# Performance work log

Hardware: AMD Instinct MI355X
Metric: run time of the kernel (lower is better)

## Reference

```python
import jax, jax.numpy as jnp
import numpy as np

H = 3  # heads
NEG_SLOPE = 0.2


def gat_conv(x, edge_index, W, a_src, a_dst, bias):
    # PyG GATConv: add self loops, per-head linear, edge attention, segment softmax over dst.
    N = x.shape[0]
    C = a_src.shape[1]
    loop = jnp.arange(N)
    src = jnp.concatenate([edge_index[0], loop])
    dst = jnp.concatenate([edge_index[1], loop])
    h = (x @ W).reshape(N, H, C)                      # [N,H,C]
    s_src = jnp.sum(h * a_src, axis=-1)               # [N,H]
    s_dst = jnp.sum(h * a_dst, axis=-1)               # [N,H]
    e = jax.nn.leaky_relu(s_src[src] + s_dst[dst], NEG_SLOPE)  # [E,H]
    m = jax.ops.segment_max(e, dst, num_segments=N)   # every node has a self loop -> finite
    e = jnp.exp(e - m[dst])
    denom = jax.ops.segment_sum(e, dst, num_segments=N)
    alpha = e / (denom[dst] + 1e-16)                  # [E,H]
    out = jax.ops.segment_sum(alpha[:, :, None] * h[src], dst, num_segments=N)  # [N,H,C]
    return out.reshape(N, H * C) + bias


def mlp(x, w1, b1, w2, b2):
    return jax.nn.gelu(x @ w1 + b1, approximate=False) @ w2 + b2


def glorot(k, shape):
    fan_in, fan_out = shape[-2], shape[-1]
    lim = np.sqrt(6.0 / (fan_in + fan_out))
    return jax.random.uniform(k, shape, jnp.float32, -lim, lim)


def setup_inputs() -> dict:
    key = jax.random.key(0)
    ks = jax.random.split(key, 24)
    N, E, F, C, HID = 50000, 800000, 256, 64, 128
    inp = {
        "x_st": jax.random.normal(ks[0], (N, F), jnp.float32),
        "edge_index_st": jax.random.randint(ks[1], (2, E), 0, N, jnp.int32),
        "x_sc": jax.random.normal(ks[2], (N, F), jnp.float32),
        "edge_index_sc": jax.random.randint(ks[3], (2, E), 0, N, jnp.int32),
    }
    for i, tag in enumerate(["st", "sc"]):
        o = 4 + i * 10
        inp[f"w_gat_{tag}"] = glorot(ks[o], (F, H * C))
        inp[f"a_src_{tag}"] = glorot(ks[o + 1], (H, C)) * 0.1
        inp[f"a_dst_{tag}"] = glorot(ks[o + 2], (H, C)) * 0.1
        inp[f"b_gat_{tag}"] = jnp.zeros((H * C,), jnp.float32)
        inp[f"w1_{tag}"] = glorot(ks[o + 3], (H * C, HID))
        inp[f"b1_{tag}"] = jnp.zeros((HID,), jnp.float32)
        inp[f"w2_{tag}"] = glorot(ks[o + 4], (HID, 1))
        inp[f"b2_{tag}"] = jnp.zeros((1,), jnp.float32)
    return inp


def reference(x_st, edge_index_st, x_sc, edge_index_sc,
              w_gat_st, a_src_st, a_dst_st, b_gat_st, w1_st, b1_st, w2_st, b2_st,
              w_gat_sc, a_src_sc, a_dst_sc, b_gat_sc, w1_sc, b1_sc, w2_sc, b2_sc):
    weight = 0.5
    h_st = jax.nn.elu(gat_conv(x_st, edge_index_st, w_gat_st, a_src_st, a_dst_st, b_gat_st))
    beta_st = mlp(h_st, w1_st, b1_st, w2_st, b2_st) / 100.0   # [N,1]
    z_st = x_st.T @ beta_st                                   # [F,1]
    h_sc = jax.nn.elu(gat_conv(x_sc, edge_index_sc, w_gat_sc, a_src_sc, a_dst_sc, b_gat_sc))
    beta_sc = mlp(h_sc, w1_sc, b1_sc, w2_sc, b2_sc) / 100.0
    z_sc = x_sc.T @ beta_sc
    out = jax.nn.sigmoid(z_sc + weight * z_st)
    return (out, beta_st, beta_sc)
```

## Files before the change

### kernel.cpp

```cpp
#include <hip/hip_runtime.h>
#include <math.h>

#define HEADS 3
#define CDIM 64
#define FDIM 256
#define HC 192
#define HIDDIM 128
#define NEG 0.2f

#define SCAN_BLK 256
#define SCAN_ELEMS 1024

#define ASTR2 40
#define BSTR 264

typedef __attribute__((ext_vector_type(8))) short short8;
typedef __attribute__((ext_vector_type(4))) float f32x4;

__device__ __forceinline__ void atomicMaxF(float* addr, float val) {
    if (val >= 0.f) atomicMax((int*)addr, __float_as_int(val));
    else            atomicMin((unsigned int*)addr, __float_as_uint(val));
}

__device__ __forceinline__ unsigned short f2bf(float f) {
    unsigned int u = __float_as_uint(f);
    u = (u + 0x7FFFu + ((u >> 16) & 1u)) >> 16;
    return (unsigned short)u;
}
__device__ __forceinline__ float bf2f(unsigned short u) {
    return __uint_as_float((unsigned int)u << 16);
}
__device__ __forceinline__ float leaky(float s) { return s >= 0.f ? s : NEG * s; }

__device__ __forceinline__ int xcd_swizzle(int orig, int nwg) {
    int q = nwg >> 3, r = nwg & 7;
    int xcd = orig & 7, idx = orig >> 3;
    return (xcd < r ? xcd * (q + 1) : r * (q + 1) + (xcd - r) * q) + idx;
}

__global__ __launch_bounds__(256) void btrans4(const float* __restrict__ wg_st,
                                               const float* __restrict__ wg_sc,
                                               const float* __restrict__ w1_st,
                                               const float* __restrict__ w1_sc,
                                               unsigned short* __restrict__ o0,
                                               unsigned short* __restrict__ o1,
                                               unsigned short* __restrict__ o2,
                                               unsigned short* __restrict__ o3) {
    int which = blockIdx.y;
    const float* src = which == 0 ? wg_st : which == 1 ? wg_sc : which == 2 ? w1_st : w1_sc;
    unsigned short* dst = which == 0 ? o0 : which == 1 ? o1 : which == 2 ? o2 : o3;
    int K  = which < 2 ? FDIM : HC;
    int Nn = which < 2 ? HC : HIDDIM;
    int total = K * Nn;
    for (int idx = blockIdx.x * 256 + threadIdx.x; idx < total; idx += gridDim.x * 256) {
        int n = idx / K, k = idx - n * K;
        dst[idx] = f2bf(src[(size_t)k * Nn + n]);
    }
}

__global__ __launch_bounds__(256) void gemm_attn(const float* __restrict__ x_st,
                                                 const float* __restrict__ x_sc,
                                                 const unsigned short* __restrict__ wgT_st,
                                                 const unsigned short* __restrict__ wgT_sc,
                                                 const float* __restrict__ as_st,
                                                 const float* __restrict__ ad_st,
                                                 const float* __restrict__ as_sc,
                                                 const float* __restrict__ ad_sc,
                                                 unsigned short* __restrict__ h_bf,
                                                 float* __restrict__ ssrc,
                                                 float* __restrict__ sdst,
                                                 int M, int nrow) {
    __shared__ unsigned short As[128 * ASTR2];
    __shared__ unsigned short Bs[64 * BSTR];
    const int nwg = nrow * HEADS * 2;
    const int wgid = xcd_swizzle(blockIdx.x, nwg);
    const int tag = wgid / (nrow * HEADS);
    const int rem = wgid - tag * (nrow * HEADS);
    const int rt = rem / HEADS;
    const int head = rem - rt * HEADS;
    const float* A = tag ? x_sc : x_st;
    const unsigned short* BT = tag ? wgT_sc : wgT_st;
    const float* a_src = tag ? as_sc : as_st;
    const float* a_dst = tag ? ad_sc : ad_st;
    const int row0 = rt * 128, col0 = head * 64;
    const int tid = threadIdx.x;
    const int wv = tid >> 6, l = tid & 63;
    const int lr = l & 15, lg = l >> 4, lk = lg * 8;
    {
        int c = tid >> 2, q = tid & 3;
        const unsigned short* bp = BT + (size_t)(col0 + c) * FDIM;
        #pragma unroll
        for (int kk = q * 8; kk < FDIM; kk += 32)
            *(short8*)(Bs + c * BSTR + kk) = *(const short8*)(bp + kk);
    }
    const int arow = tid >> 1, aseg = tid & 1;
    const int gr = row0 + arow;
    f32x4 acc[2][4] = {};
    for (int ks = 0; ks < FDIM / 32; ++ks) {
        int k0 = ks * 32;
        short8 av1 = {0,0,0,0,0,0,0,0}, av2 = {0,0,0,0,0,0,0,0};
        if (gr < M) {
            const float* p = A + (size_t)gr * FDIM + k0 + aseg * 16;
            float4 x0 = *(const float4*)p;
            float4 x1 = *(const float4*)(p + 4);
            float4 x2 = *(const float4*)(p + 8);
            float4 x3 = *(const float4*)(p + 12);
            av1[0] = (short)f2bf(x0.x); av1[1] = (short)f2bf(x0.y);
            av1[2] = (short)f2bf(x0.z); av1[3] = (short)f2bf(x0.w);
            av1[4] = (short)f2bf(x1.x); av1[5] = (short)f2bf(x1.y);
            av1[6] = (short)f2bf(x1.z); av1[7] = (short)f2bf(x1.w);
            av2[0] = (short)f2bf(x2.x); av2[1] = (short)f2bf(x2.y);
            av2[2] = (short)f2bf(x2.z); av2[3] = (short)f2bf(x2.w);
            av2[4] = (short)f2bf(x3.x); av2[5] = (short)f2bf(x3.y);
            av2[6] = (short)f2bf(x3.z); av2[7] = (short)f2bf(x3.w);
        }
        *(short8*)(As + arow * ASTR2 + aseg * 16) = av1;
        *(short8*)(As + arow * ASTR2 + aseg * 16 + 8) = av2;
        __syncthreads();
        #pragma unroll
        for (int m = 0; m < 2; ++m) {
            short8 af = *(const short8*)(As + (wv * 32 + m * 16 + lr) * ASTR2 + lk);
            #pragma unroll
            for (int nb = 0; nb < 4; ++nb) {
                short8 bfm = *(const short8*)(Bs + (nb * 16 + lr) * BSTR + k0 + lk);
                acc[m][nb] = __builtin_amdgcn_mfma_f32_16x16x32_bf16(af, bfm, acc[m][nb], 0, 0, 0);
            }
        }
        __syncthreads();
    }
    const size_t tagbase = (size_t)tag * M;
    #pragma unroll
    for (int m = 0; m < 2; ++m)
        #pragma unroll
        for (int nb = 0; nb < 4; ++nb)
            #pragma unroll
            for (int r = 0; r < 4; ++r) {
                int grow = row0 + wv * 32 + m * 16 + lg * 4 + r;
                if (grow < M)
                    h_bf[(tagbase + grow) * HC + col0 + nb * 16 + lr] = f2bf(acc[m][nb][r]);
            }
    float avs[4], avd[4];
    #pragma unroll
    for (int nb = 0; nb < 4; ++nb) {
        avs[nb] = a_src[col0 + nb * 16 + lr];
        avd[nb] = a_dst[col0 + nb * 16 + lr];
    }
    #pragma unroll
    for (int m = 0; m < 2; ++m)
        #pragma unroll
        for (int r = 0; r < 4; ++r) {
            float ds = acc[m][0][r] * avs[0] + acc[m][1][r] * avs[1]
                     + acc[m][2][r] * avs[2] + acc[m][3][r] * avs[3];
            float dd = acc[m][0][r] * avd[0] + acc[m][1][r] * avd[1]
                     + acc[m][2][r] * avd[2] + acc[m][3][r] * avd[3];
            #pragma unroll
            for (int off = 8; off; off >>= 1) {
                ds += __shfl_down(ds, off);
                dd += __shfl_down(dd, off);
            }
            int grow = row0 + wv * 32 + m * 16 + lg * 4 + r;
            if (lr == 0 && grow < M) {
                ssrc[(tagbase + grow) * 3 + head] = ds;
                sdst[(tagbase + grow) * 3 + head] = dd;
            }
        }
}

__global__ __launch_bounds__(256) void prep(const int* __restrict__ ei_st,
                                            const int* __restrict__ ei_sc,
                                            int* __restrict__ deg,
                                            const float* __restrict__ ssrc,
                                            const float* __restrict__ sdst,
                                            float* __restrict__ gmax,
                                            int N, int E, int Etot) {
    if (blockIdx.y < 2) {
        int e = blockIdx.x * 256 + threadIdx.x;
        if (e >= Etot) return;
        const int* ei = blockIdx.y ? ei_sc : ei_st;
        int dst = (e < E) ? ei[E + e] : (e - E);
        atomicAdd(&deg[blockIdx.y * N + dst], 1);
        return;
    }
    if (blockIdx.x >= 32) return;
    __shared__ float red[4][12];
    float v[12];
    #pragma unroll
    for (int j = 0; j < 12; ++j) v[j] = -1e30f;
    const int stride = 32 * 256;
    for (int n = blockIdx.x * 256 + threadIdx.x; n < 2 * N; n += stride) {
        float s0 = ssrc[n * 3], s1 = ssrc[n * 3 + 1], s2 = ssrc[n * 3 + 2];
        float d0 = sdst[n * 3], d1 = sdst[n * 3 + 1], d2 = sdst[n * 3 + 2];
        if (n < N) {
            v[0] = fmaxf(v[0], s0); v[1] = fmaxf(v[1], s1); v[2] = fmaxf(v[2], s2);
            v[3] = fmaxf(v[3], d0); v[4] = fmaxf(v[4], d1); v[5] = fmaxf(v[5], d2);
        } else {
            v[6] = fmaxf(v[6], s0); v[7] = fmaxf(v[7], s1); v[8] = fmaxf(v[8], s2);
            v[9] = fmaxf(v[9], d0); v[10] = fmaxf(v[10], d1); v[11] = fmaxf(v[11], d2);
        }
    }
    #pragma unroll
    for (int j = 0; j < 12; ++j)
        #pragma unroll
        for (int off = 32; off; off >>= 1)
            v[j] = fmaxf(v[j], __shfl_down(v[j], off));
    int wave = threadIdx.x >> 6, lane = threadIdx.x & 63;
    if (lane == 0) {
        #pragma unroll
        for (int j = 0; j < 12; ++j) red[wave][j] = v[j];
    }
    __syncthreads();
    if (threadIdx.x < 12) {
        float m = fmaxf(fmaxf(red[0][threadIdx.x], red[1][threadIdx.x]),
                        fmaxf(red[2][threadIdx.x], red[3][threadIdx.x]));
        atomicMaxF(&gmax[threadIdx.x], m);
    }
}

__global__ __launch_bounds__(SCAN_BLK) void scan1(const int* __restrict__ deg,
                                                  int* __restrict__ row_ptr,
                                                  int* __restrict__ bsums, int N2) {
    __shared__ int sm[SCAN_BLK];
    int tid = threadIdx.x;
    int base = blockIdx.x * SCAN_ELEMS + tid * 4;
    int v[4];
    #pragma unroll
    for (int j = 0; j < 4; ++j) v[j] = (base + j < N2) ? deg[base + j] : 0;
    int tsum = v[0] + v[1] + v[2] + v[3];
    sm[tid] = tsum;
    __syncthreads();
    for (int off = 1; off < SCAN_BLK; off <<= 1) {
        int y = (tid >= off) ? sm[tid - off] : 0;
        __syncthreads();
        sm[tid] += y;
        __syncthreads();
    }
    int run = sm[tid] - tsum;
    #pragma unroll
    for (int j = 0; j < 4; ++j) {
        if (base + j < N2) row_ptr[base + j] = run;
        run += v[j];
    }
    if (tid == SCAN_BLK - 1) bsums[blockIdx.x] = sm[SCAN_BLK - 1];
}

__global__ __launch_bounds__(SCAN_BLK) void scan2(int* __restrict__ bsums, int nb) {
    __shared__ int sm[SCAN_BLK];
    int tid = threadIdx.x;
    int v = (tid < nb) ? bsums[tid] : 0;
    sm[tid] = v;
    __syncthreads();
    for (int off = 1; off < SCAN_BLK; off <<= 1) {
        int y = (tid >= off) ? sm[tid - off] : 0;
        __syncthreads();
        sm[tid] += y;
        __syncthreads();
    }
    if (tid < nb) bsums[tid] = sm[tid] - v;
}

__global__ __launch_bounds__(256) void scatter_p2(const int* __restrict__ ei_st,
                                                  const int* __restrict__ ei_sc,
                                                  const float* __restrict__ s_src_all,
                                                  const float* __restrict__ s_dst_all,
                                                  const float* __restrict__ gmax,
                                                  const int* __restrict__ row_ptr,
                                                  const int* __restrict__ bsums,
                                                  int* __restrict__ cursor,
                                                  float4* __restrict__ csr_data,
                                                  int N, int E, int Etot) {
    int e = blockIdx.x * blockDim.x + threadIdx.x;
    if (e >= Etot) return;
    const int tag = blockIdx.y;
    const int* ei = tag ? ei_sc : ei_st;
    const float* s_src = s_src_all + (size_t)tag * N * 3;
    const float* s_dst = s_dst_all + (size_t)tag * N * 3;
    const float* gm = gmax + tag * 6;
    int src, dst;
    if (e < E) { src = ei[e]; dst = ei[E + e]; } else { src = dst = e - E; }
    float M0 = leaky(gm[0] + gm[3]);
    float M1 = leaky(gm[1] + gm[4]);
    float M2 = leaky(gm[2] + gm[5]);
    float p0 = __expf(leaky(s_src[src * 3 + 0] + s_dst[dst * 3 + 0]) - M0);
    float p1 = __expf(leaky(s_src[src * 3 + 1] + s_dst[dst * 3 + 1]) - M1);
    float p2 = __expf(leaky(s_src[src * 3 + 2] + s_dst[dst * 3 + 2]) - M2);
    int g = tag * N + dst;
    int pos = row_ptr[g] + bsums[g >> 10] + atomicAdd(&cursor[g], 1);
    csr_data[pos] = make_float4(__int_as_float(tag * N + src), p0, p1, p2);
}

__global__ __launch_bounds__(256) void csr_agg2(const int* __restrict__ row_ptr,
                                                const int* __restrict__ bsums,
                                                const int* __restrict__ deg,
                                                const float4* __restrict__ csr_data,
                                                const unsigned short* __restrict__ Hall,
                                                const float* __restrict__ bias_st,
                                                const float* __restrict__ bias_sc,
                                                unsigned short* __restrict__ og, int N) {
    int gid = blockIdx.x * blockDim.x + threadIdx.x;
    int node = gid >> 6, lane = gid & 63;
    if (node >= 2 * N) return;
    const float* bias = (node >= N) ? bias_sc : bias_st;
    int start = row_ptr[node] + bsums[node >> 10];
    int cnt = deg[node];
    float acc0 = 0.f, acc1 = 0.f, acc2 = 0.f;
    float d0 = 0.f, d1 = 0.f, d2 = 0.f;
    int i = 0;
    for (; i + 3 < cnt; i += 4) {
        float4 v0 = csr_data[start + i];
        float4 v1 = csr_data[start + i + 1];
        float4 v2 = csr_data[start + i + 2];
        float4 v3 = csr_data[start + i + 3];
        const unsigned short* r0 =
            Hall + (size_t)__builtin_amdgcn_readfirstlane(__float_as_int(v0.x)) * HC + lane;
        const unsigned short* r1 =
            Hall + (size_t)__builtin_amdgcn_readfirstlane(__float_as_int(v1.x)) * HC + lane;
        const unsigned short* r2 =
            Hall + (size_t)__builtin_amdgcn_readfirstlane(__float_as_int(v2.x)) * HC + lane;
        const unsigned short* r3 =
            Hall + (size_t)__builtin_amdgcn_readfirstlane(__float_as_int(v3.x)) * HC + lane;
        float h00 = bf2f(r0[0]), h01 = bf2f(r0[64]), h02 = bf2f(r0[128]);
        float h10 = bf2f(r1[0]), h11 = bf2f(r1[64]), h12 = bf2f(r1[128]);
        float h20 = bf2f(r2[0]), h21 = bf2f(r2[64]), h22 = bf2f(r2[128]);
        float h30 = bf2f(r3[0]), h31 = bf2f(r3[64]), h32 = bf2f(r3[128]);
        acc0 = fmaf(v0.y, h00, acc0); acc1 = fmaf(v0.z, h01, acc1); acc2 = fmaf(v0.w, h02, acc2);
        acc0 = fmaf(v1.y, h10, acc0); acc1 = fmaf(v1.z, h11, acc1); acc2 = fmaf(v1.w, h12, acc2);
        acc0 = fmaf(v2.y, h20, acc0); acc1 = fmaf(v2.z, h21, acc1); acc2 = fmaf(v2.w, h22, acc2);
        acc0 = fmaf(v3.y, h30, acc0); acc1 = fmaf(v3.z, h31, acc1); acc2 = fmaf(v3.w, h32, acc2);
        d0 += (v0.y + v1.y) + (v2.y + v3.y);
        d1 += (v0.z + v1.z) + (v2.z + v3.z);
        d2 += (v0.w + v1.w) + (v2.w + v3.w);
    }
    for (; i < cnt; ++i) {
        float4 v0 = csr_data[start + i];
        const unsigned short* r0 =
            Hall + (size_t)__builtin_amdgcn_readfirstlane(__float_as_int(v0.x)) * HC + lane;
        acc0 = fmaf(v0.y, bf2f(r0[0]),   acc0);
        acc1 = fmaf(v0.z, bf2f(r0[64]),  acc1);
        acc2 = fmaf(v0.w, bf2f(r0[128]), acc2);
        d0 += v0.y; d1 += v0.z; d2 += v0.w;
    }
    float o0 = acc0 / (d0 + 1e-16f) + bias[lane];
    float o1 = acc1 / (d1 + 1e-16f) + bias[64 + lane];
    float o2 = acc2 / (d2 + 1e-16f) + bias[128 + lane];
    o0 = o0 > 0.f ? o0 : expm1f(o0);
    o1 = o1 > 0.f ? o1 : expm1f(o1);
    o2 = o2 > 0.f ? o2 : expm1f(o2);
    unsigned short* orow = og + (size_t)node * HC + lane;
    orow[0] = f2bf(o0); orow[64] = f2bf(o1); orow[128] = f2bf(o2);
}

__global__ __launch_bounds__(256) void gemm_beta(const unsigned short* __restrict__ og_bf,
                                                 const unsigned short* __restrict__ w1T_st,
                                                 const unsigned short* __restrict__ w1T_sc,
                                                 const float* __restrict__ b1_st,
                                                 const float* __restrict__ w2_st,
                                                 const float* __restrict__ b2_st,
                                                 const float* __restrict__ b1_sc,
                                                 const float* __restrict__ w2_sc,
                                                 const float* __restrict__ b2_sc,
                                                 float* __restrict__ beta_out,
                                                 int M, int nrow) {
    __shared__ unsigned short As[128 * ASTR2];
    __shared__ unsigned short Bs[64 * BSTR];
    const int nwg = nrow * 2 * 2;
    const int wgid = xcd_swizzle(blockIdx.x, nwg);
    const int tag = wgid / (nrow * 2);
    const int rem = wgid - tag * (nrow * 2);
    const int rt = rem >> 1;
    const int ct = rem & 1;
    const unsigned short* A = og_bf + (size_t)tag * M * HC;
    const unsigned short* BT = tag ? w1T_sc : w1T_st;
    const float* b1 = tag ? b1_sc : b1_st;
    const float* w2 = tag ? w2_sc : w2_st;
    const float b2h = (tag ? b2_sc : b2_st)[0] * 0.005f;
    const int row0 = rt * 128, col0 = ct * 64;
    const int tid = threadIdx.x;
    const int wv = tid >> 6, l = tid & 63;
    const int lr = l & 15, lg = l >> 4, lk = lg * 8;
    {
        int c = tid >> 2, q = tid & 3;
        const unsigned short* bp = BT + (size_t)(col0 + c) * HC;
        #pragma unroll
        for (int kk = q * 8; kk < HC; kk += 32)
            *(short8*)(Bs + c * BSTR + kk) = *(const short8*)(bp + kk);
    }
    const int arow = tid >> 1, aseg = tid & 1;
    const int gr = row0 + arow;
    f32x4 acc[2][4] = {};
    for (int ks = 0; ks < HC / 32; ++ks) {
        int k0 = ks * 32;
        short8 av1 = {0,0,0,0,0,0,0,0}, av2 = {0,0,0,0,0,0,0,0};
        if (gr < M) {
            const unsigned short* p = A + (size_t)gr * HC + k0 + aseg * 16;
            av1 = *(const short8*)p;
            av2 = *(const short8*)(p + 8);
        }
        *(short8*)(As + arow * ASTR2 + aseg * 16) = av1;
        *(short8*)(As + arow * ASTR2 + aseg * 16 + 8) = av2;
        __syncthreads();
        #pragma unroll
        for (int m = 0; m < 2; ++m) {
            short8 af = *(const short8*)(As + (wv * 32 + m * 16 + lr) * ASTR2 + lk);
            #pragma unroll
            for (int nb = 0; nb < 4; ++nb) {
                short8 bfm = *(const short8*)(Bs + (nb * 16 + lr) * BSTR + k0 + lk);
                acc[m][nb] = __builtin_amdgcn_mfma_f32_16x16x32_bf16(af, bfm, acc[m][nb], 0, 0, 0);
            }
        }
        __syncthreads();
    }
    float b1v[4], w2v[4];
    #pragma unroll
    for (int nb = 0; nb < 4; ++nb) {
        b1v[nb] = b1[col0 + nb * 16 + lr];
        w2v[nb] = w2[col0 + nb * 16 + lr];
    }
    #pragma unroll
    for (int m = 0; m < 2; ++m)
        #pragma unroll
        for (int r = 0; r < 4; ++r) {
            float p = 0.f;
            #pragma unroll
            for (int nb = 0; nb < 4; ++nb) {
                float vx = acc[m][nb][r] + b1v[nb];
                float g = 0.5f * vx * (1.f + erff(vx * 0.70710678118654752f));
                p = fmaf(g, w2v[nb], p);
            }
            #pragma unroll
            for (int off = 8; off; off >>= 1) p += __shfl_down(p, off);
            int grow = row0 + wv * 32 + m * 16 + lg * 4 + r;
            if (lr == 0 && grow < M)
                atomicAdd(&beta_out[(size_t)tag * M + grow], p * 0.01f + b2h);
        }
}

__global__ __launch_bounds__(256) void xt_beta2(const float* __restrict__ X_st,
                                                const float* __restrict__ X_sc,
                                                const float* __restrict__ beta_all,
                                                float* __restrict__ z_all, int N) {
    const int tag = blockIdx.y;
    const float* X = tag ? X_sc : X_st;
    const float* beta = beta_all + (size_t)tag * N;
    float* z = z_all + tag * FDIM;
    int f = threadIdx.x;
    int nPer = (N + gridDim.x - 1) / gridDim.x;
    int n0 = blockIdx.x * nPer;
    int n1 = min(n0 + nPer, N);
    float acc = 0.f;
    for (int n = n0; n < n1; ++n)
        acc = fmaf(X[(size_t)n * FDIM + f], beta[n], acc);
    atomicAdd(&z[f], acc);
}

__global__ void final_sigmoid(const float* __restrict__ z_all,
                              float* __restrict__ out) {
    int f = threadIdx.x;
    float v = z_all[FDIM + f] + 0.5f * z_all[f];
    out[f] = 1.f / (1.f + expf(-v));
}

extern "C" void kernel_launch(void* const* d_in, const int* in_sizes, int n_in,
                              void* d_out, int out_size, void* d_ws, size_t ws_size,
                              hipStream_t stream) {
    const float* x_st = (const float*)d_in[0];
    const int*   ei_st = (const int*)d_in[1];
    const float* x_sc = (const float*)d_in[2];
    const int*   ei_sc = (const int*)d_in[3];
    const int N = in_sizes[0] / FDIM;
    const int E = in_sizes[1] / 2;
    const int Etot = E + N;
    const int N2 = 2 * N;

    const float* wg_st   = (const float*)d_in[4];
    const float* asrc_st = (const float*)d_in[5];
    const float* adst_st = (const float*)d_in[6];
    const float* bg_st   = (const float*)d_in[7];
    const float* w1_st   = (const float*)d_in[8];
    const float* b1_st   = (const float*)d_in[9];
    const float* w2_st   = (const float*)d_in[10];
    const float* b2_st   = (const float*)d_in[11];
    const float* wg_sc   = (const float*)d_in[12];
    const float* asrc_sc = (const float*)d_in[13];
    const float* adst_sc = (const float*)d_in[14];
    const float* bg_sc   = (const float*)d_in[15];
    const float* w1_sc   = (const float*)d_in[16];
    const float* b1_sc   = (const float*)d_in[17];
    const float* w2_sc   = (const float*)d_in[18];
    const float* b2_sc   = (const float*)d_in[19];

    float* out = (float*)d_out;
    float* beta_out = out + FDIM;

    char* wp = (char*)d_ws;
    auto alloc = [&](size_t bytes) { char* r = wp; wp += (bytes + 63) & ~(size_t)63; return r; };
    int*   degb   = (int*)alloc(((size_t)2 * N2 + 16 + 512) * 4);
    int*   cursor = degb + N2;
    float* gmax   = (float*)(cursor + N2);
    float* zbuf   = gmax + 16;
    size_t zero_bytes = ((size_t)2 * N2 + 16 + 512) * 4;

    unsigned short* h_bf  = (unsigned short*)alloc((size_t)N2 * HC * 2);
    unsigned short* og_bf = (unsigned short*)alloc((size_t)N2 * HC * 2);
    float4*         csr_data = (float4*)alloc((size_t)2 * Etot * 16);
    float* ssrc = (float*)alloc((size_t)N2 * 3 * 4);
    float* sdst = (float*)alloc((size_t)N2 * 3 * 4);
    int* row_ptr = (int*)alloc((size_t)N2 * 4);
    int* bsums   = (int*)alloc(SCAN_BLK * 4);
    unsigned short* wgT_st = (unsigned short*)alloc((size_t)HC * FDIM * 2);
    unsigned short* wgT_sc = (unsigned short*)alloc((size_t)HC * FDIM * 2);
    unsigned short* w1T_st = (unsigned short*)alloc((size_t)HIDDIM * HC * 2);
    unsigned short* w1T_sc = (unsigned short*)alloc((size_t)HIDDIM * HC * 2);

    const int nb_scan = (N2 + SCAN_ELEMS - 1) / SCAN_ELEMS;
    const int nrow_t = (N + 127) / 128;

    hipMemsetAsync(degb, 0, zero_bytes, stream);
    hipMemsetAsync(d_out, 0, (size_t)out_size * 4, stream);

    btrans4<<<dim3(96, 4), 256, 0, stream>>>(wg_st, wg_sc, w1_st, w1_sc,
                                             wgT_st, wgT_sc, w1T_st, w1T_sc);

    gemm_attn<<<nrow_t * HEADS * 2, 256, 0, stream>>>(
        x_st, x_sc, wgT_st, wgT_sc, asrc_st, adst_st, asrc_sc, adst_sc,
        h_bf, ssrc, sdst, N, nrow_t);

    prep<<<dim3((Etot + 255) / 256, 3), 256, 0, stream>>>(ei_st, ei_sc, degb,
                                                          ssrc, sdst, gmax, N, E, Etot);

    scan1<<<nb_scan, SCAN_BLK, 0, stream>>>(degb, row_ptr, bsums, N2);
    scan2<<<1, SCAN_BLK, 0, stream>>>(bsums, nb_scan);

    scatter_p2<<<dim3((Etot + 255) / 256, 2), 256, 0, stream>>>(
        ei_st, ei_sc, ssrc, sdst, gmax, row_ptr, bsums, cursor, csr_data, N, E, Etot);

    csr_agg2<<<(N2 + 3) / 4, 256, 0, stream>>>(row_ptr, bsums, degb, csr_data, h_bf,
                                               bg_st, bg_sc, og_bf, N);

    gemm_beta<<<nrow_t * 2 * 2, 256, 0, stream>>>(og_bf, w1T_st, w1T_sc,
                                                  b1_st, w2_st, b2_st,
                                                  b1_sc, w2_sc, b2_sc, beta_out, N, nrow_t);

    xt_beta2<<<dim3(512, 2), 256, 0, stream>>>(x_st, x_sc, beta_out, zbuf, N);

    final_sigmoid<<<1, FDIM, 0, stream>>>(zbuf, out);
}
```

Measured before the change: 390.1 us.

## Fuse memsets into setup kernel, widen beta GEMM tile, fold sigmoid, nontemporal CSR

Replaces the two memsets with a zeroing slice inside the weight-transpose kernel. The beta GEMM now covers all 128 hidden columns per block, so it writes beta directly instead of combining column halves with atomics. The final sigmoid kernel is merged into the xt_beta reduction using a last-block-done counter. CSR edge records are also stored and loaded with nontemporal hints. Together these cut launch overhead and atomics, at the cost of more registers and LDS in the GEMM and a grid-wide completion flag.

```diff
diff --git a/kernel.cpp b/kernel.cpp
--- a/kernel.cpp
+++ b/kernel.cpp
@@ -13,6 +13,7 @@
 
 #define ASTR2 40
 #define BSTR 264
+#define BSTRB 200
 
 typedef __attribute__((ext_vector_type(8))) short short8;
 typedef __attribute__((ext_vector_type(4))) float f32x4;
@@ -38,15 +39,21 @@
     return (xcd < r ? xcd * (q + 1) : r * (q + 1) + (xcd - r) * q) + idx;
 }
 
-__global__ __launch_bounds__(256) void btrans4(const float* __restrict__ wg_st,
-                                               const float* __restrict__ wg_sc,
-                                               const float* __restrict__ w1_st,
-                                               const float* __restrict__ w1_sc,
-                                               unsigned short* __restrict__ o0,
-                                               unsigned short* __restrict__ o1,
-                                               unsigned short* __restrict__ o2,
-                                               unsigned short* __restrict__ o3) {
+__global__ __launch_bounds__(256) void setup(const float* __restrict__ wg_st,
+                                             const float* __restrict__ wg_sc,
+                                             const float* __restrict__ w1_st,
+                                             const float* __restrict__ w1_sc,
+                                             unsigned short* __restrict__ o0,
+                                             unsigned short* __restrict__ o1,
+                                             unsigned short* __restrict__ o2,
+                                             unsigned short* __restrict__ o3,
+                                             int* __restrict__ zero_base, int zero_ints) {
     int which = blockIdx.y;
+    if (which == 4) {
+        for (int i = blockIdx.x * 256 + threadIdx.x; i < zero_ints; i += gridDim.x * 256)
+            zero_base[i] = 0;
+        return;
+    }
     const float* src = which == 0 ? wg_st : which == 1 ? wg_sc : which == 2 ? w1_st : w1_sc;
     unsigned short* dst = which == 0 ? o0 : which == 1 ? o1 : which == 2 ? o2 : o3;
     int K  = which < 2 ? FDIM : HC;
@@ -266,7 +273,7 @@
                                                   const int* __restrict__ row_ptr,
                                                   const int* __restrict__ bsums,
                                                   int* __restrict__ cursor,
-                                                  float4* __restrict__ csr_data,
+                                                  f32x4* __restrict__ csr_data,
                                                   int N, int E, int Etot) {
     int e = blockIdx.x * blockDim.x + threadIdx.x;
     if (e >= Etot) return;
@@ -285,13 +292,14 @@
     float p2 = __expf(leaky(s_src[src * 3 + 2] + s_dst[dst * 3 + 2]) - M2);
     int g = tag * N + dst;
     int pos = row_ptr[g] + bsums[g >> 10] + atomicAdd(&cursor[g], 1);
-    csr_data[pos] = make_float4(__int_as_float(tag * N + src), p0, p1, p2);
+    f32x4 val = {__int_as_float(tag * N + src), p0, p1, p2};
+    __builtin_nontemporal_store(val, &csr_data[pos]);
 }
 
 __global__ __launch_bounds__(256) void csr_agg2(const int* __restrict__ row_ptr,
                                                 const int* __restrict__ bsums,
                                                 const int* __restrict__ deg,
-                                                const float4* __restrict__ csr_data,
+                                                const f32x4* __restrict__ csr_data,
                                                 const unsigned short* __restrict__ Hall,
                                                 const float* __restrict__ bias_st,
                                                 const float* __restrict__ bias_sc,
@@ -306,38 +314,38 @@
     float d0 = 0.f, d1 = 0.f, d2 = 0.f;
     int i = 0;
     for (; i + 3 < cnt; i += 4) {
-        float4 v0 = csr_data[start + i];
-        float4 v1 = csr_data[start + i + 1];
-        float4 v2 = csr_data[start + i + 2];
-        float4 v3 = csr_data[start + i + 3];
+        f32x4 v0 = __builtin_nontemporal_load(&csr_data[start + i]);
+        f32x4 v1 = __builtin_nontemporal_load(&csr_data[start + i + 1]);
+        f32x4 v2 = __builtin_nontemporal_load(&csr_data[start + i + 2]);
+        f32x4 v3 = __builtin_nontemporal_load(&csr_data[start + i + 3]);
         const unsigned short* r0 =
-            Hall + (size_t)__builtin_amdgcn_readfirstlane(__float_as_int(v0.x)) * HC + lane;
+            Hall + (size_t)__builtin_amdgcn_readfirstlane(__float_as_int(v0[0])) * HC + lane;
         const unsigned short* r1 =
-            Hall + (size_t)__builtin_amdgcn_readfirstlane(__float_as_int(v1.x)) * HC + lane;
+            Hall + (size_t)__builtin_amdgcn_readfirstlane(__float_as_int(v1[0])) * HC + lane;
         const unsigned short* r2 =
-            Hall + (size_t)__builtin_amdgcn_readfirstlane(__float_as_int(v2.x)) * HC + lane;
+            Hall + (size_t)__builtin_amdgcn_readfirstlane(__float_as_int(v2[0])) * HC + lane;
         const unsigned short* r3 =
-            Hall + (size_t)__builtin_amdgcn_readfirstlane(__float_as_int(v3.x)) * HC + lane;
+            Hall + (size_t)__builtin_amdgcn_readfirstlane(__float_as_int(v3[0])) * HC + lane;
         float h00 = bf2f(r0[0]), h01 = bf2f(r0[64]), h02 = bf2f(r0[128]);
         float h10 = bf2f(r1[0]), h11 = bf2f(r1[64]), h12 = bf2f(r1[128]);
         float h20 = bf2f(r2[0]), h21 = bf2f(r2[64]), h22 = bf2f(r2[128]);
         float h30 = bf2f(r3[0]), h31 = bf2f(r3[64]), h32 = bf2f(r3[128]);
-        acc0 = fmaf(v0.y, h00, acc0); acc1 = fmaf(v0.z, h01, acc1); acc2 = fmaf(v0.w, h02, acc2);
-        acc0 = fmaf(v1.y, h10, acc0); acc1 = fmaf(v1.z, h11, acc1); acc2 = fmaf(v1.w, h12, acc2);
-        acc0 = fmaf(v2.y, h20, acc0); acc1 = fmaf(v2.z, h21, acc1); acc2 = fmaf(v2.w, h22, acc2);
-        acc0 = fmaf(v3.y, h30, acc0); acc1 = fmaf(v3.z, h31, acc1); acc2 = fmaf(v3.w, h32, acc2);
-        d0 += (v0.y + v1.y) + (v2.y + v3.y);
-        d1 += (v0.z + v1.z) + (v2.z + v3.z);
-        d2 += (v0.w + v1.w) + (v2.w + v3.w);
+        acc0 = fmaf(v0[1], h00, acc0); acc1 = fmaf(v0[2], h01, acc1); acc2 = fmaf(v0[3], h02, acc2);
+        acc0 = fmaf(v1[1], h10, acc0); acc1 = fmaf(v1[2], h11, acc1); acc2 = fmaf(v1[3], h12, acc2);
+        acc0 = fmaf(v2[1], h20, acc0); acc1 = fmaf(v2[2], h21, acc1); acc2 = fmaf(v2[3], h22, acc2);
+        acc0 = fmaf(v3[1], h30, acc0); acc1 = fmaf(v3[2], h31, acc1); acc2 = fmaf(v3[3], h32, acc2);
+        d0 += (v0[1] + v1[1]) + (v2[1] + v3[1]);
+        d1 += (v0[2] + v1[2]) + (v2[2] + v3[2]);
+        d2 += (v0[3] + v1[3]) + (v2[3] + v3[3]);
     }
     for (; i < cnt; ++i) {
-        float4 v0 = csr_data[start + i];
+        f32x4 v0 = __builtin_nontemporal_load(&csr_data[start + i]);
         const unsigned short* r0 =
-            Hall + (size_t)__builtin_amdgcn_readfirstlane(__float_as_int(v0.x)) * HC + lane;
-        acc0 = fmaf(v0.y, bf2f(r0[0]),   acc0);
-        acc1 = fmaf(v0.z, bf2f(r0[64]),  acc1);
-        acc2 = fmaf(v0.w, bf2f(r0[128]), acc2);
-        d0 += v0.y; d1 += v0.z; d2 += v0.w;
+            Hall + (size_t)__builtin_amdgcn_readfirstlane(__float_as_int(v0[0])) * HC + lane;
+        acc0 = fmaf(v0[1], bf2f(r0[0]),   acc0);
+        acc1 = fmaf(v0[2], bf2f(r0[64]),  acc1);
+        acc2 = fmaf(v0[3], bf2f(r0[128]), acc2);
+        d0 += v0[1]; d1 += v0[2]; d2 += v0[3];
     }
     float o0 = acc0 / (d0 + 1e-16f) + bias[lane];
     float o1 = acc1 / (d1 + 1e-16f) + bias[64 + lane];
@@ -361,32 +369,32 @@
                                                  float* __restrict__ beta_out,
                                                  int M, int nrow) {
     __shared__ unsigned short As[128 * ASTR2];
-    __shared__ unsigned short Bs[64 * BSTR];
-    const int nwg = nrow * 2 * 2;
+    __shared__ unsigned short Bs[128 * BSTRB];
+    const int nwg = nrow * 2;
     const int wgid = xcd_swizzle(blockIdx.x, nwg);
-    const int tag = wgid / (nrow * 2);
-    const int rem = wgid - tag * (nrow * 2);
-    const int rt = rem >> 1;
-    const int ct = rem & 1;
+    const int tag = wgid / nrow;
+    const int rt = wgid - tag * nrow;
     const unsigned short* A = og_bf + (size_t)tag * M * HC;
     const unsigned short* BT = tag ? w1T_sc : w1T_st;
     const float* b1 = tag ? b1_sc : b1_st;
     const float* w2 = tag ? w2_sc : w2_st;
-    const float b2h = (tag ? b2_sc : b2_st)[0] * 0.005f;
-    const int row0 = rt * 128, col0 = ct * 64;
+    const float b2v = (tag ? b2_sc : b2_st)[0];
+    const int row0 = rt * 128;
     const int tid = threadIdx.x;
     const int wv = tid >> 6, l = tid & 63;
     const int lr = l & 15, lg = l >> 4, lk = lg * 8;
     {
-        int c = tid >> 2, q = tid & 3;
-        const unsigned short* bp = BT + (size_t)(col0 + c) * HC;
-        #pragma unroll
-        for (int kk = q * 8; kk < HC; kk += 32)
-            *(short8*)(Bs + c * BSTR + kk) = *(const short8*)(bp + kk);
+        int c = tid >> 1, half = tid & 1;
+        const unsigned short* bp = BT + (size_t)c * HC;
+        #pragma unroll
+        for (int j = 0; j < 12; ++j) {
+            int kk = half * 96 + j * 8;
+            *(short8*)(Bs + c * BSTRB + kk) = *(const short8*)(bp + kk);
+        }
     }
     const int arow = tid >> 1, aseg = tid & 1;
     const int gr = row0 + arow;
-    f32x4 acc[2][4] = {};
+    f32x4 acc[2][8] = {};
     for (int ks = 0; ks < HC / 32; ++ks) {
         int k0 = ks * 32;
         short8 av1 = {0,0,0,0,0,0,0,0}, av2 = {0,0,0,0,0,0,0,0};
@@ -402,18 +410,18 @@
         for (int m = 0; m < 2; ++m) {
             short8 af = *(const short8*)(As + (wv * 32 + m * 16 + lr) * ASTR2 + lk);
             #pragma unroll
-            for (int nb = 0; nb < 4; ++nb) {
-                short8 bfm = *(const short8*)(Bs + (nb * 16 + lr) * BSTR + k0 + lk);
+            for (int nb = 0; nb < 8; ++nb) {
+                short8 bfm = *(const short8*)(Bs + (nb * 16 + lr) * BSTRB + k0 + lk);
                 acc[m][nb] = __builtin_amdgcn_mfma_f32_16x16x32_bf16(af, bfm, acc[m][nb], 0, 0, 0);
             }
         }
         __syncthreads();
     }
-    float b1v[4], w2v[4];
-    #pragma unroll
-    for (int nb = 0; nb < 4; ++nb) {
-        b1v[nb] = b1[col0 + nb * 16 + lr];
-        w2v[nb] = w2[col0 + nb * 16 + lr];
+    float b1v[8], w2v[8];
+    #pragma unroll
+    for (int nb = 0; nb < 8; ++nb) {
+        b1v[nb] = b1[nb * 16 + lr];
+        w2v[nb] = w2[nb * 16 + lr];
     }
     #pragma unroll
     for (int m = 0; m < 2; ++m)
@@ -421,7 +429,7 @@
         for (int r = 0; r < 4; ++r) {
             float p = 0.f;
             #pragma unroll
-            for (int nb = 0; nb < 4; ++nb) {
+            for (int nb = 0; nb < 8; ++nb) {
                 float vx = acc[m][nb][r] + b1v[nb];
                 float g = 0.5f * vx * (1.f + erff(vx * 0.70710678118654752f));
                 p = fmaf(g, w2v[nb], p);
@@ -430,14 +438,16 @@
             for (int off = 8; off; off >>= 1) p += __shfl_down(p, off);
             int grow = row0 + wv * 32 + m * 16 + lg * 4 + r;
             if (lr == 0 && grow < M)
-                atomicAdd(&beta_out[(size_t)tag * M + grow], p * 0.01f + b2h);
-        }
-}
-
-__global__ __launch_bounds__(256) void xt_beta2(const float* __restrict__ X_st,
-                                                const float* __restrict__ X_sc,
-                                                const float* __restrict__ beta_all,
-                                                float* __restrict__ z_all, int N) {
+                beta_out[(size_t)tag * M + grow] = (p + b2v) * 0.01f;
+        }
+}
+
+__global__ __launch_bounds__(256) void xt_beta_final(const float* __restrict__ X_st,
+                                                     const float* __restrict__ X_sc,
+                                                     const float* __restrict__ beta_all,
+                                                     float* __restrict__ z_all,
+                                                     int* __restrict__ flag,
+                                                     float* __restrict__ out, int N) {
     const int tag = blockIdx.y;
     const float* X = tag ? X_sc : X_st;
     const float* beta = beta_all + (size_t)tag * N;
@@ -450,13 +460,20 @@
     for (int n = n0; n < n1; ++n)
         acc = fmaf(X[(size_t)n * FDIM + f], beta[n], acc);
     atomicAdd(&z[f], acc);
-}
-
-__global__ void final_sigmoid(const float* __restrict__ z_all,
-                              float* __restrict__ out) {
-    int f = threadIdx.x;
-    float v = z_all[FDIM + f] + 0.5f * z_all[f];
-    out[f] = 1.f / (1.f + expf(-v));
+    __threadfence();
+    __syncthreads();
+    __shared__ int isLast;
+    if (f == 0) {
+        int old = atomicAdd(flag, 1);
+        isLast = (old == (int)(gridDim.x * gridDim.y) - 1);
+    }
+    __syncthreads();
+    if (isLast) {
+        float zst = atomicAdd(&z_all[f], 0.f);
+        float zsc = atomicAdd(&z_all[FDIM + f], 0.f);
+        float v = zsc + 0.5f * zst;
+        out[f] = 1.f / (1.f + expf(-v));
+    }
 }
 
 extern "C" void kernel_launch(void* const* d_in, const int* in_sizes, int n_in,
@@ -493,15 +510,16 @@
 
     char* wp = (char*)d_ws;
     auto alloc = [&](size_t bytes) { char* r = wp; wp += (bytes + 63) & ~(size_t)63; return r; };
-    int*   degb   = (int*)alloc(((size_t)2 * N2 + 16 + 512) * 4);
+    const int zero_ints = 2 * N2 + 16 + 512 + 16;
+    int*   degb   = (int*)alloc((size_t)zero_ints * 4);
     int*   cursor = degb + N2;
     float* gmax   = (float*)(cursor + N2);
     float* zbuf   = gmax + 16;
-    size_t zero_bytes = ((size_t)2 * N2 + 16 + 512) * 4;
+    int*   flag   = (int*)(zbuf + 512);
 
     unsigned short* h_bf  = (unsigned short*)alloc((size_t)N2 * HC * 2);
     unsigned short* og_bf = (unsigned short*)alloc((size_t)N2 * HC * 2);
-    float4*         csr_data = (float4*)alloc((size_t)2 * Etot * 16);
+    f32x4*          csr_data = (f32x4*)alloc((size_t)2 * Etot * 16);
     float* ssrc = (float*)alloc((size_t)N2 * 3 * 4);
     float* sdst = (float*)alloc((size_t)N2 * 3 * 4);
     int* row_ptr = (int*)alloc((size_t)N2 * 4);
@@ -514,11 +532,9 @@
     const int nb_scan = (N2 + SCAN_ELEMS - 1) / SCAN_ELEMS;
     const int nrow_t = (N + 127) / 128;
 
-    hipMemsetAsync(degb, 0, zero_bytes, stream);
-    hipMemsetAsync(d_out, 0, (size_t)out_size * 4, stream);
-
-    btrans4<<<dim3(96, 4), 256, 0, stream>>>(wg_st, wg_sc, w1_st, w1_sc,
-                                             wgT_st, wgT_sc, w1T_st, w1T_sc);
+    setup<<<dim3(96, 5), 256, 0, stream>>>(wg_st, wg_sc, w1_st, w1_sc,
+                                           wgT_st, wgT_sc, w1T_st, w1T_sc,
+                                           degb, zero_ints);
 
     gemm_attn<<<nrow_t * HEADS * 2, 256, 0, stream>>>(
         x_st, x_sc, wgT_st, wgT_sc, asrc_st, adst_st, asrc_sc, adst_sc,
@@ -536,11 +552,10 @@
     csr_agg2<<<(N2 + 3) / 4, 256, 0, stream>>>(row_ptr, bsums, degb, csr_data, h_bf,
                                                bg_st, bg_sc, og_bf, N);
 
-    gemm_beta<<<nrow_t * 2 * 2, 256, 0, stream>>>(og_bf, w1T_st, w1T_sc,
-                                                  b1_st, w2_st, b2_st,
-                                                  b1_sc, w2_sc, b2_sc, beta_out, N, nrow_t);
-
-    xt_beta2<<<dim3(512, 2), 256, 0, stream>>>(x_st, x_sc, beta_out, zbuf, N);
-
-    final_sigmoid<<<1, FDIM, 0, stream>>>(zbuf, out);
-}
+    gemm_beta<<<nrow_t * 2, 256, 0, stream>>>(og_bf, w1T_st, w1T_sc,
+                                              b1_st, w2_st, b2_st,
+                                              b1_sc, w2_sc, b2_sc, beta_out, N, nrow_t);
+
+    xt_beta_final<<<dim3(512, 2), 256, 0, stream>>>(x_st, x_sc, beta_out, zbuf,
+                                                    flag, out, N);
+}
```

Result: slower. 458.8 us (+17.6%).
